# Performance work log

Measured on AMD Instinct MI355X. Metric: run time of the kernel, lower is better.

The kernel has to match this reference:

```python
import jax, jax.numpy as jnp
import numpy as np

# --- boolean gate helpers on {0,1}-valued float pulses ---
def OR(a, b):
    return a + b - a * b

def AND(a, b):
    return a * b

def NOT(a):
    return 1.0 - a

def XOR(a, b):
    return a + b - 2.0 * a * b

def MUX(sel, a, b):
    # sel ? a : b (broadcasts sel over last dim)
    return sel * a + (1.0 - sel) * b


def setup_inputs() -> dict:
    key = jax.random.key(0)
    shape = (8192, 2048, 8)
    fp8_pulse = (jax.random.uniform(key, shape) < 0.5).astype(jnp.float32)
    return {"fp8_pulse": fp8_pulse}


def reference(fp8_pulse):
    batch_shape = fp8_pulse.shape[:-1]
    dt = fp8_pulse.dtype
    zeros = jnp.zeros(batch_shape + (1,), dtype=dt)
    ones = jnp.ones(batch_shape + (1,), dtype=dt)

    s  = fp8_pulse[..., 0:1]
    e3 = fp8_pulse[..., 1:2]
    e2 = fp8_pulse[..., 2:3]
    e1 = fp8_pulse[..., 3:4]
    e0 = fp8_pulse[..., 4:5]
    m2 = fp8_pulse[..., 5:6]
    m1 = fp8_pulse[..., 6:7]
    m0 = fp8_pulse[..., 7:8]

    e_nonzero = OR(OR(e0, e1), OR(e2, e3))
    e_is_zero = NOT(e_nonzero)
    m_nonzero = OR(OR(m0, m1), m2)
    is_subnormal = AND(e_is_zero, m_nonzero)

    # 5-bit ripple-carry adder (LSB-first): fp8_exp + 8
    a_bits = [e0, e1, e2, e3, zeros]
    b_bits = [zeros, zeros, zeros, ones, zeros]  # const 8, LSB-first
    carry = zeros
    sum_bits = []
    for i in range(5):
        axb = XOR(a_bits[i], b_bits[i])
        sum_bits.append(XOR(axb, carry))
        carry = OR(AND(a_bits[i], b_bits[i]), AND(carry, axb))
    # MSB-first FP16 exponent for the normal case
    fp16_exp_normal = jnp.concatenate(sum_bits[::-1], axis=-1)

    fp16_mant_normal = jnp.concatenate([m2, m1, m0] + [zeros] * 7, axis=-1)

    # leading-one detection for subnormal FP8
    lead_at_2 = m2
    lead_at_1 = AND(NOT(m2), m1)
    lead_at_0 = AND(AND(NOT(m2), NOT(m1)), m0)
    _ = lead_at_1  # kept for faithfulness; not used downstream (as in original)

    exp_8 = jnp.concatenate([zeros, ones, zeros, zeros, zeros], axis=-1)
    exp_7 = jnp.concatenate([zeros, zeros, ones, ones, ones], axis=-1)
    exp_6 = jnp.concatenate([zeros, zeros, ones, ones, zeros], axis=-1)

    sub_exp_01 = MUX(lead_at_0, exp_6, exp_7)
    sub_exp = MUX(lead_at_2, exp_8, sub_exp_01)

    mant_lead2 = jnp.concatenate([m1, m0] + [zeros] * 8, axis=-1)
    mant_lead1 = jnp.concatenate([m0] + [zeros] * 9, axis=-1)
    mant_lead0 = jnp.concatenate([zeros] * 10, axis=-1)

    sub_mant_01 = MUX(lead_at_0, mant_lead0, mant_lead1)
    sub_mant = MUX(lead_at_2, mant_lead2, sub_mant_01)

    is_zero = AND(e_is_zero, NOT(m_nonzero))
    not_is_zero = NOT(is_zero)

    fp16_exp = AND(MUX(is_subnormal, sub_exp, fp16_exp_normal), not_is_zero)
    fp16_mant = AND(MUX(is_subnormal, sub_mant, fp16_mant_normal), not_is_zero)

    return jnp.concatenate([s, fp16_exp, fp16_mant], axis=-1)
```

## Files before the change

kernel.cpp:

```cpp
#include <hip/hip_runtime.h>
#include <cstdint>


__global__ __launch_bounds__(256) void fp8_to_fp16_bits_kernel(
    const float4* __restrict__ in4,
    float4* __restrict__ out4,
    int n_out4)
{
    int idx = blockIdx.x * blockDim.x + threadIdx.x;
    int stride = gridDim.x * blockDim.x;
    for (int o = idx; o < n_out4; o += stride) {
        int g = o >> 2;
        int q = o & 3;
        float4 a = in4[2 * g];
        float4 b = in4[2 * g + 1];

        uint32_t s  = a.x != 0.0f;
        uint32_t e3 = a.y != 0.0f;
        uint32_t e2 = a.z != 0.0f;
        uint32_t e1 = a.w != 0.0f;
        uint32_t e0 = b.x != 0.0f;
        uint32_t m2 = b.y != 0.0f;
        uint32_t m1 = b.z != 0.0f;
        uint32_t m0 = b.w != 0.0f;

        uint32_t e = (e3 << 3) | (e2 << 2) | (e1 << 1) | e0;
        uint32_t m = (m2 << 2) | (m1 << 1) | m0;

        uint32_t exp5  = e  ? e + 8u
                       : m2 ? 8u
                       : m1 ? 7u
                       : m0 ? 6u
                       :      0u;
        uint32_t mant10 = e  ? (m << 7)
                        : m2 ? ((m & 3u) << 8)
                        : m1 ? ((m & 1u) << 9)
                        :      0u;

        uint32_t word = (s << 15) | (exp5 << 10) | mant10;

        int sh = 15 - 4 * q;
        float4 r;
        r.x = ((word >> (sh    )) & 1u) ? 1.0f : 0.0f;
        r.y = ((word >> (sh - 1)) & 1u) ? 1.0f : 0.0f;
        r.z = ((word >> (sh - 2)) & 1u) ? 1.0f : 0.0f;
        r.w = ((word >> (sh - 3)) & 1u) ? 1.0f : 0.0f;

        out4[o] = r;
    }
}

extern "C" void kernel_launch(void* const* d_in, const int* in_sizes, int n_in,
                              void* d_out, int out_size, void* d_ws, size_t ws_size,
                              hipStream_t stream)
{
    const float4* in4 = (const float4*)d_in[0];
    float4* out4 = (float4*)d_out;
    int n_out4 = out_size / 4;

    dim3 grid(2048), block(256);
    fp8_to_fp16_bits_kernel<<<grid, block, 0, stream>>>(in4, out4, n_out4);
}
```

Baseline: 1.366 ms.

## Load each input group once per lane and distribute output words via wave shuffles

Before, each output float4 re-read both input float4s, so every input group was loaded four times. Now each lane loads one group once, computes the FP16 word, and broadcasts it with __shfl so four coalesced float4 stores per lane cover the outputs. Loads and stores also become nontemporal, to keep this streaming data from polluting the caches. The cost is extra cross-lane shuffles, and the loop no longer has a tail guard for group counts that are not multiples of 64.

```diff
diff --git a/kernel.cpp b/kernel.cpp
--- a/kernel.cpp
+++ b/kernel.cpp
@@ -2,51 +2,58 @@
 #include <cstdint>
 
 
+typedef float f32x4 __attribute__((ext_vector_type(4)));
+
 __global__ __launch_bounds__(256) void fp8_to_fp16_bits_kernel(
-    const float4* __restrict__ in4,
-    float4* __restrict__ out4,
-    int n_out4)
+    const f32x4* __restrict__ in4,
+    f32x4* __restrict__ out4,
+    int n_groups)
 {
-    int idx = blockIdx.x * blockDim.x + threadIdx.x;
-    int stride = gridDim.x * blockDim.x;
-    for (int o = idx; o < n_out4; o += stride) {
-        int g = o >> 2;
-        int q = o & 3;
-        float4 a = in4[2 * g];
-        float4 b = in4[2 * g + 1];
+    const int lane   = threadIdx.x & 63;
+    const int gwave  = (int)((blockIdx.x * blockDim.x + threadIdx.x) >> 6);
+    const int nwaves = (int)((gridDim.x * blockDim.x) >> 6);
+    const int q    = lane & 3;
+    const int sh3  = 12 - 4 * q;
+    const int srcb = lane >> 2;
 
-        uint32_t s  = a.x != 0.0f;
-        uint32_t e3 = a.y != 0.0f;
-        uint32_t e2 = a.z != 0.0f;
-        uint32_t e1 = a.w != 0.0f;
-        uint32_t e0 = b.x != 0.0f;
-        uint32_t m2 = b.y != 0.0f;
-        uint32_t m1 = b.z != 0.0f;
-        uint32_t m0 = b.w != 0.0f;
+    for (int base = gwave * 64; base < n_groups; base += nwaves * 64) {
+        const int g = base + lane;
+        f32x4 a = __builtin_nontemporal_load(&in4[2 * g]);
+        f32x4 b = __builtin_nontemporal_load(&in4[2 * g + 1]);
+
+        uint32_t s  = a[0] != 0.0f;
+        uint32_t e3 = a[1] != 0.0f;
+        uint32_t e2 = a[2] != 0.0f;
+        uint32_t e1 = a[3] != 0.0f;
+        uint32_t e0 = b[0] != 0.0f;
+        uint32_t m2 = b[1] != 0.0f;
+        uint32_t m1 = b[2] != 0.0f;
+        uint32_t m0 = b[3] != 0.0f;
 
         uint32_t e = (e3 << 3) | (e2 << 2) | (e1 << 1) | e0;
         uint32_t m = (m2 << 2) | (m1 << 1) | m0;
 
-        uint32_t exp5  = e  ? e + 8u
-                       : m2 ? 8u
-                       : m1 ? 7u
-                       : m0 ? 6u
-                       :      0u;
-        uint32_t mant10 = e  ? (m << 7)
-                        : m2 ? ((m & 3u) << 8)
-                        : m1 ? ((m & 1u) << 9)
-                        :      0u;
+        uint32_t exp5 = e  ? e + 8u
+                      : m2 ? 8u
+                      : m1 ? 7u
+                      : m0 ? 6u
+                      :      0u;
+        uint32_t mant = e  ? (m << 7)
+                      : m2 ? ((m & 3u) << 8)
+                      : m1 ? ((m & 1u) << 9)
+                      :      0u;
+        uint32_t word = (s << 15) | (exp5 << 10) | mant;
 
-        uint32_t word = (s << 15) | (exp5 << 10) | mant10;
-
-        int sh = 15 - 4 * q;
-        float4 r;
-        r.x = ((word >> (sh    )) & 1u) ? 1.0f : 0.0f;
-        r.y = ((word >> (sh - 1)) & 1u) ? 1.0f : 0.0f;
-        r.z = ((word >> (sh - 2)) & 1u) ? 1.0f : 0.0f;
-        r.w = ((word >> (sh - 3)) & 1u) ? 1.0f : 0.0f;
-
-        out4[o] = r;
+        #pragma unroll
+        for (int k = 0; k < 4; ++k) {
+            uint32_t w = (uint32_t)__shfl((int)word, 16 * k + srcb, 64);
+            f32x4 r;
+            r[0] = (float)((w >> (sh3 + 3)) & 1u);
+            r[1] = (float)((w >> (sh3 + 2)) & 1u);
+            r[2] = (float)((w >> (sh3 + 1)) & 1u);
+            r[3] = (float)((w >> (sh3    )) & 1u);
+            __builtin_nontemporal_store(r, &out4[4 * base + 64 * k + lane]);
+        }
     }
 }
 
@@ -54,10 +61,10 @@
                               void* d_out, int out_size, void* d_ws, size_t ws_size,
                               hipStream_t stream)
 {
-    const float4* in4 = (const float4*)d_in[0];
-    float4* out4 = (float4*)d_out;
-    int n_out4 = out_size / 4;
+    const f32x4* in4 = (const f32x4*)d_in[0];
+    f32x4* out4 = (f32x4*)d_out;
+    int n_groups = in_sizes[0] / 8;
 
     dim3 grid(2048), block(256);
-    fp8_to_fp16_bits_kernel<<<grid, block, 0, stream>>>(in4, out4, n_out4);
+    fp8_to_fp16_bits_kernel<<<grid, block, 0, stream>>>(in4, out4, n_groups);
 }
```

After: 1.351 ms. No clear change (-1.1%).
